# Kernel optimization log

Hardware: AMD Instinct MI355X
Metric: run time of the kernel (lower is better)

## Reference

```python
import jax, jax.numpy as jnp
import numpy as np

B, N, DIN, DOUT, H, DH, DC, NL, L = 8, 256, 64, 64, 8, 8, 64, 32, 2
SCALE = DH ** -0.5  # out_dim-per-head scaling used by both attention variants


def _ln(x, g, b):
    m = jnp.mean(x, -1, keepdims=True)
    v = jnp.mean((x - m) ** 2, -1, keepdims=True)
    return (x - m) * jax.lax.rsqrt(v + 1e-5) * g + b


def _cross_attn(x, ctx, mask_b, wq, wkv, wo, bo):
    # CrossAttentionLayer: standard softmax attention with clamp(-5,5)
    b, n, _ = x.shape
    m = ctx.shape[1]
    q = (x @ wq).reshape(b, n, H, DH).transpose(0, 2, 1, 3)
    k, v = jnp.split(ctx @ wkv, 2, axis=-1)
    k = k.reshape(b, m, H, DH).transpose(0, 2, 1, 3)
    v = v.reshape(b, m, H, DH).transpose(0, 2, 1, 3)
    sim = jnp.einsum('bhid,bhjd->bhij', q, k) * SCALE
    if mask_b is not None:
        sim = jnp.where(mask_b[:, None, None, :], sim, -jnp.finfo(sim.dtype).max)
    sim = jnp.clip(sim, -5.0, 5.0)
    attn = jax.nn.softmax(sim, axis=-1)
    out = jnp.einsum('bhij,bhjd->bhid', attn, v)
    out = out.transpose(0, 2, 1, 3).reshape(b, n, H * DH)
    return out @ wo + bo


def _mha_edge(p, e, k_RW, mask, wq, wk, we, wv):
    # GraphiT MultiHeadAttentionLayer with edge features + k_RW attention PE
    Q = (p @ wq).reshape(B, N, H, DH)
    K = (p @ wk).reshape(B, N, H, DH) * SCALE
    V = (p @ wv).reshape(B, N, H, DH).transpose(0, 2, 1, 3)  # [B,H,N,d]
    E = (e @ we).reshape(B, N, N, H, DH)
    scores = jnp.einsum('bihk,bjhk,bijhk->bhij', Q, K, E)
    scores = jnp.exp(scores - jnp.max(scores, axis=(-2, -1), keepdims=True))
    scores = scores * mask[:, None, :, None] * mask[:, None, None, :]
    scores = scores * k_RW
    denom = jnp.clip(jnp.sum(scores, -1, keepdims=True), 1e-6, None)
    out = jnp.einsum('bhij,bhjd->bhid', scores, V) / denom
    return out.transpose(0, 2, 1, 3).reshape(B, N, H * DH)


def setup_inputs() -> dict:
    key = jax.random.key(0)
    ks = jax.random.split(key, 32)
    rn = lambda k, s: jax.random.normal(k, s, dtype=jnp.float32)
    inp = {
        'h': rn(ks[0], (B, N, DIN)),
        'p': rn(ks[1], (B, N, DIN)),
        'e': rn(ks[2], (B, N, N, DIN)),
        'k_RW': jax.random.uniform(ks[3], (B, 1, N, N), dtype=jnp.float32),
        'queries': rn(ks[4], (B, NL, DC)),
        'mask': jnp.ones((B, N), dtype=jnp.float32),
        # attention_p (MultiHeadAttentionLayer) weights
        'wq_p': rn(ks[5], (DIN, H * DH)) * 0.05,
        'wk_p': rn(ks[6], (DIN, H * DH)) * 0.05,
        'we_p': rn(ks[7], (DIN, H * DH)) * 0.05,
        'wv_p': rn(ks[8], (DIN, H * DH)) * 0.05,
        'wo_p': rn(ks[9], (DOUT, DOUT)) * 0.05,
        # cross_attention_h (queries attend to nodes)
        'cq_wq': rn(ks[10], (DC, H * DH)) * 0.05,
        'cq_wkv': rn(ks[11], (DIN, 2 * H * DH)) * 0.05,
        'cq_wo': rn(ks[12], (H * DH, DC)) * 0.05,
        'cq_bo': jnp.zeros((DC,), dtype=jnp.float32),
        # L_cross latent self-attention layers (stacked)
        'sa_wq': rn(ks[13], (L, DC, H * DH)) * 0.05,
        'sa_wkv': rn(ks[14], (L, DC, 2 * H * DH)) * 0.05,
        'sa_wo': rn(ks[15], (L, H * DH, DC)) * 0.05,
        'sa_bo': jnp.zeros((L, DC), dtype=jnp.float32),
        # O_queries, norms, FFN
        'oq_w': rn(ks[16], (DC, DC)) * 0.05,
        'ln1_g': jnp.ones((DC,), dtype=jnp.float32),
        'ln1_b': jnp.zeros((DC,), dtype=jnp.float32),
        'ffn_w1': rn(ks[17], (DC, 2 * DC)) * 0.05,
        'ffn_w2': rn(ks[18], (2 * DC, DC)) * 0.05,
        'ln2_g': jnp.ones((DC,), dtype=jnp.float32),
        'ln2_b': jnp.zeros((DC,), dtype=jnp.float32),
    }
    return inp


def reference(h, p, e, k_RW, queries, mask,
              wq_p, wk_p, we_p, wv_p, wo_p,
              cq_wq, cq_wkv, cq_wo, cq_bo,
              sa_wq, sa_wkv, sa_wo, sa_bo,
              oq_w, ln1_g, ln1_b, ffn_w1, ffn_w2, ln2_g, ln2_b):
    # forward_p: update positional encoding via edge-modulated attention
    p_attn = _mha_edge(p, e, k_RW, mask, wq_p, wk_p, we_p, wv_p)
    p_new = p + jnp.tanh(p_attn @ wo_p)  # residual, no dropout (eval)
    # combine node features with updated PE (use_node_pe='sum')
    h_c = h + p_new
    mask_b = mask > 0.5
    # perceiver cross-attention: latents attend to nodes
    q = queries + _cross_attn(queries, h_c, mask_b, cq_wq, cq_wkv, cq_wo, cq_bo)
    # L_cross latent self-attention blocks with residual
    for i in range(L):
        q = q + _cross_attn(q, q, None, sa_wq[i], sa_wkv[i], sa_wo[i], sa_bo[i])
    # O_queries projection + layer norm
    q = _ln(q @ oq_w, ln1_g, ln1_b)
    # feed-forward block on queries
    ff = jax.nn.relu(q @ ffn_w1) @ ffn_w2
    q = _ln(q + ff, ln2_g, ln2_b)
    return q
```

## Files before the change

kernel.cpp:

```cpp
#include <hip/hip_runtime.h>
#include <hip/hip_bf16.h>
#include <math.h>

typedef __bf16 bf16x8 __attribute__((ext_vector_type(8)));
typedef float floatx4 __attribute__((ext_vector_type(4)));

#define ATT_SCALE 0.35355339059327373f

__device__ __forceinline__ __bf16 f2b(float x) { return (__bf16)x; }

__global__ void k_proj(const float* __restrict__ p, const float* __restrict__ quer,
                       const float* __restrict__ wq, const float* __restrict__ wk,
                       const float* __restrict__ wv, const float* __restrict__ cq_wq,
                       float* __restrict__ Q, float* __restrict__ Ks,
                       float* __restrict__ V, float* __restrict__ q1) {
  int blk = blockIdx.x, t = threadIdx.x;
  __shared__ float xr[64];
  if (blk < 2048) {
    xr[t] = p[blk * 64 + t];
    __syncthreads();
    float aq = 0.f, ak = 0.f, av = 0.f;
    for (int c = 0; c < 64; c++) {
      float x = xr[c];
      aq += x * wq[c * 64 + t];
      ak += x * wk[c * 64 + t];
      av += x * wv[c * 64 + t];
    }
    Q[blk * 64 + t] = aq;
    Ks[blk * 64 + t] = ak * ATT_SCALE;
    V[blk * 64 + t] = av;
  } else {
    int r = blk - 2048;
    xr[t] = quer[r * 64 + t];
    __syncthreads();
    float a = 0.f;
    for (int c = 0; c < 64; c++) a += xr[c] * cq_wq[c * 64 + t];
    q1[r * 64 + t] = a;
  }
}

#define LOADT(ER, JT) do {                         \
    const float* _np = ebase + (JT) * 1024;        \
    ER[0] = *(const float4*)(_np);                 \
    ER[1] = *(const float4*)(_np + 4);             \
    ER[2] = *(const float4*)(_np + 32);            \
    ER[3] = *(const float4*)(_np + 36);            \
  } while (0)

#define NTCOMP(NT, KF, VA) do {                                               \
    floatx4 acc = {0.f, 0.f, 0.f, 0.f};                                       \
    acc = __builtin_amdgcn_mfma_f32_16x16x32_bf16(wfrag[NT][0], a0, acc, 0, 0, 0); \
    acc = __builtin_amdgcn_mfma_f32_16x16x32_bf16(wfrag[NT][1], a1, acc, 0, 0, 0); \
    float s = acc[0] * KF.x * qv[NT].x + acc[1] * KF.y * qv[NT].y +           \
              acc[2] * KF.z * qv[NT].z + acc[3] * KF.w * qv[NT].w;            \
    s += __shfl_xor(s, 16);                                                   \
    float wg = __expf(s) * kwm;                                               \
    aden[NT] += wg;                                                           \
    aout[NT][0] += wg * VA.x; aout[NT][1] += wg * VA.y;                       \
    aout[NT][2] += wg * VA.z; aout[NT][3] += wg * VA.w;                       \
  } while (0)

#define STEP(JT, ER, PFSTMT) do {                                             \
    int jS = w * 64 + (JT) * 16 + l15;                                        \
    const float* ksrow = Ks + ((long)(b * 256 + jS)) * 64 + quad * 4;         \
    const float* vrow  = V  + ((long)(b * 256 + jS)) * 64 + hsel * 8 + par * 4; \
    float4 kf0 = *(const float4*)(ksrow);                                     \
    float4 kf1 = *(const float4*)(ksrow + 16);                                \
    float4 kf2 = *(const float4*)(ksrow + 32);                                \
    float4 kf3 = *(const float4*)(ksrow + 48);                                \
    float4 va0 = *(const float4*)(vrow);                                      \
    float4 va1 = *(const float4*)(vrow + 16);                                 \
    float4 va2 = *(const float4*)(vrow + 32);                                 \
    float4 va3 = *(const float4*)(vrow + 48);                                 \
    float kwm = krw[(long)bi * 256 + jS] * mask[b * 256 + jS];                \
    __builtin_amdgcn_sched_barrier(0);                                        \
    PFSTMT;                                                                   \
    __builtin_amdgcn_sched_barrier(0);                                        \
    bf16x8 a0, a1;                                                            \
    a0[0] = f2b(ER[0].x); a0[1] = f2b(ER[0].y);                               \
    a0[2] = f2b(ER[0].z); a0[3] = f2b(ER[0].w);                               \
    a0[4] = f2b(ER[1].x); a0[5] = f2b(ER[1].y);                               \
    a0[6] = f2b(ER[1].z); a0[7] = f2b(ER[1].w);                               \
    a1[0] = f2b(ER[2].x); a1[1] = f2b(ER[2].y);                               \
    a1[2] = f2b(ER[2].z); a1[3] = f2b(ER[2].w);                               \
    a1[4] = f2b(ER[3].x); a1[5] = f2b(ER[3].y);                               \
    a1[6] = f2b(ER[3].z); a1[7] = f2b(ER[3].w);                               \
    NTCOMP(0, kf0, va0); NTCOMP(1, kf1, va1);                                 \
    NTCOMP(2, kf2, va2); NTCOMP(3, kf3, va3);                                 \
  } while (0)

__global__ __launch_bounds__(256, 1) void k_edge(
    const float* __restrict__ e, const float* __restrict__ we,
    const float* __restrict__ krw, const float* __restrict__ mask,
    const float* __restrict__ hin, const float* __restrict__ pin,
    const float* __restrict__ wo, const float* __restrict__ cq_wkv,
    const float* __restrict__ Q, const float* __restrict__ Ks,
    const float* __restrict__ V, float* __restrict__ Kc, float* __restrict__ Vc) {
  int bi = blockIdx.x;
  int b = bi >> 8;
  int t = threadIdx.x;
  int w = t >> 6, l = t & 63;
  int l15 = l & 15, quad = l >> 4;
  int hsel = quad >> 1;
  int par = quad & 1;

  bf16x8 wfrag[4][2];
#pragma unroll
  for (int nt = 0; nt < 4; nt++)
#pragma unroll
    for (int kc = 0; kc < 2; kc++)
#pragma unroll
      for (int jj = 0; jj < 8; jj++)
        wfrag[nt][kc][jj] = f2b(we[(kc * 32 + quad * 8 + jj) * 64 + nt * 16 + l15]);

  float4 qv[4];
#pragma unroll
  for (int nt = 0; nt < 4; nt++)
    qv[nt] = *(const float4*)(Q + bi * 64 + nt * 16 + quad * 4);

  float mi = mask[bi];

  float aout[4][4];
  float aden[4] = {0.f, 0.f, 0.f, 0.f};
#pragma unroll
  for (int nt = 0; nt < 4; nt++)
#pragma unroll
    for (int d = 0; d < 4; d++) aout[nt][d] = 0.f;

  const float* ebase = e + ((long)bi * 256 + w * 64 + l15) * 64 + quad * 8;

  float4 e0[4], e1[4], e2[4], e3[4];
  LOADT(e0, 0);
  LOADT(e1, 1);
  LOADT(e2, 2);
  __builtin_amdgcn_sched_barrier(0);

  STEP(0, e0, LOADT(e3, 3));
  STEP(1, e1, (void)0);
  STEP(2, e2, (void)0);
  STEP(3, e3, (void)0);

#pragma unroll
  for (int nt = 0; nt < 4; nt++) {
    float dn = aden[nt];
    dn += __shfl_xor(dn, 1); dn += __shfl_xor(dn, 2);
    dn += __shfl_xor(dn, 4); dn += __shfl_xor(dn, 8);
    aden[nt] = dn;
#pragma unroll
    for (int d = 0; d < 4; d++) {
      float o = aout[nt][d];
      o += __shfl_xor(o, 1); o += __shfl_xor(o, 2);
      o += __shfl_xor(o, 4); o += __shfl_xor(o, 8);
      aout[nt][d] = o;
    }
  }

  __shared__ float red[4][64];
  __shared__ float redden[4][8];
  __shared__ float pav[64];
  __shared__ float hcl[64];
  if (l15 == 0) {
#pragma unroll
    for (int nt = 0; nt < 4; nt++) {
      int head = nt * 2 + hsel;
#pragma unroll
      for (int d = 0; d < 4; d++) red[w][head * 8 + par * 4 + d] = aout[nt][d];
      if (par == 0) redden[w][head] = aden[nt];
    }
  }
  __syncthreads();
  if (t < 64) {
    int head = t >> 3;
    float num = red[0][t] + red[1][t] + red[2][t] + red[3][t];
    float den = redden[0][head] + redden[1][head] + redden[2][head] + redden[3][head];
    num *= mi;
    den = fmaxf(den * mi, 1e-6f);
    pav[t] = num / den;
  }
  __syncthreads();
  if (t < 64) {
    float a = 0.f;
    for (int c = 0; c < 64; c++) a += pav[c] * wo[c * 64 + t];
    hcl[t] = hin[bi * 64 + t] + pin[bi * 64 + t] + tanhf(a);
  }
  __syncthreads();
  if (t < 128) {
    float a = 0.f;
    for (int c = 0; c < 64; c++) a += hcl[c] * cq_wkv[c * 128 + t];
    if (t < 64) Kc[bi * 64 + t] = a;
    else        Vc[bi * 64 + t - 64] = a;
  }
}

__global__ __launch_bounds__(256) void k_crossf(
    const float* __restrict__ q1, const float* __restrict__ Kc,
    const float* __restrict__ Vc, const float* __restrict__ mask,
    const float* __restrict__ quer, const float* __restrict__ cq_wo,
    const float* __restrict__ cq_bo, const float* __restrict__ wq0,
    const float* __restrict__ wkv0, float* __restrict__ q0g,
    float* __restrict__ qqg, float* __restrict__ kvg) {
  int blk = blockIdx.x, b = blk >> 3, rg = blk & 7;
  int t = threadIdx.x, rr = t >> 6, l = t & 63, h = l >> 3, g = l & 7;
  int gr = b * 32 + rg * 4 + rr;
  __shared__ float ocs[4][64];
  __shared__ float q0s[4][64];

  {
    const float* qp = q1 + gr * 64 + h * 8;
    float4 qa = *(const float4*)qp, qb = *(const float4*)(qp + 4);
    float num[8] = {0.f, 0.f, 0.f, 0.f, 0.f, 0.f, 0.f, 0.f};
    float den = 0.f;
#pragma unroll 4
    for (int jj = 0; jj < 32; jj++) {
      int j = jj * 8 + g;
      const float* kp = Kc + (b * 256 + j) * 64 + h * 8;
      float4 ka = *(const float4*)kp, kb = *(const float4*)(kp + 4);
      float s = qa.x * ka.x + qa.y * ka.y + qa.z * ka.z + qa.w * ka.w +
                qb.x * kb.x + qb.y * kb.y + qb.z * kb.z + qb.w * kb.w;
      s *= ATT_SCALE;
      float mj = mask[b * 256 + j];
      s = (mj > 0.5f) ? s : -1e30f;
      s = fminf(fmaxf(s, -5.f), 5.f);
      float ex = __expf(s);
      den += ex;
      const float* vp = Vc + (b * 256 + j) * 64 + h * 8;
      float4 va = *(const float4*)vp, vb = *(const float4*)(vp + 4);
      num[0] += ex * va.x; num[1] += ex * va.y;
      num[2] += ex * va.z; num[3] += ex * va.w;
      num[4] += ex * vb.x; num[5] += ex * vb.y;
      num[6] += ex * vb.z; num[7] += ex * vb.w;
    }
    den += __shfl_xor(den, 1); den += __shfl_xor(den, 2); den += __shfl_xor(den, 4);
#pragma unroll
    for (int d = 0; d < 8; d++) {
      float v = num[d];
      v += __shfl_xor(v, 1); v += __shfl_xor(v, 2); v += __shfl_xor(v, 4);
      num[d] = v;
    }
    float sel = num[0];
#pragma unroll
    for (int d = 1; d < 8; d++) sel = (g == d) ? num[d] : sel;
    ocs[rr][h * 8 + g] = sel / den;
  }

  int c = l;
  {
    float acc = quer[gr * 64 + c] + cq_bo[c];
    for (int k = 0; k < 64; k++) acc += ocs[rr][k] * cq_wo[k * 64 + c];
    q0g[gr * 64 + c] = acc;
    q0s[rr][c] = acc;
  }
  {
    float aq = 0.f, ak = 0.f, av = 0.f;
    for (int k = 0; k < 64; k++) {
      float x = q0s[rr][k];
      aq += x * wq0[k * 64 + c];
      ak += x * wkv0[k * 128 + c];
      av += x * wkv0[k * 128 + 64 + c];
    }
    qqg[gr * 64 + c] = aq;
    kvg[gr * 128 + c] = ak;
    kvg[gr * 128 + 64 + c] = av;
  }
}

__global__ __launch_bounds__(256) void k_sattnf(
    const float* __restrict__ qq, const float* __restrict__ kv,
    const float* __restrict__ resid, const float* __restrict__ wo,
    const float* __restrict__ bo, const float* __restrict__ wq2,
    const float* __restrict__ wkv2, float* __restrict__ q_out,
    float* __restrict__ qq2, float* __restrict__ kv2) {
  int blk = blockIdx.x, b = blk >> 3, rg = blk & 7;
  int t = threadIdx.x, rr = t >> 6, l = t & 63, h = l >> 3, g = l & 7;
  int gr = b * 32 + rg * 4 + rr;
  __shared__ float KVs[32][128];
  __shared__ float ocs[4][64];
  __shared__ float q2s[4][64];

  const float4* s4 = (const float4*)(kv + b * 4096);
  float4* d4 = (float4*)&KVs[0][0];
#pragma unroll
  for (int i = 0; i < 4; i++) d4[i * 256 + t] = s4[i * 256 + t];

  const float* qp = qq + gr * 64 + h * 8;
  float4 qa = *(const float4*)qp, qb = *(const float4*)(qp + 4);
  __syncthreads();

  {
    float num[8] = {0.f, 0.f, 0.f, 0.f, 0.f, 0.f, 0.f, 0.f};
    float den = 0.f;
#pragma unroll
    for (int jj = 0; jj < 4; jj++) {
      int j = jj * 8 + g;
      float4 ka = *(const float4*)&KVs[j][h * 8];
      float4 kb = *(const float4*)&KVs[j][h * 8 + 4];
      float s = qa.x * ka.x + qa.y * ka.y + qa.z * ka.z + qa.w * ka.w +
                qb.x * kb.x + qb.y * kb.y + qb.z * kb.z + qb.w * kb.w;
      s *= ATT_SCALE;
      s = fminf(fmaxf(s, -5.f), 5.f);
      float ex = __expf(s);
      den += ex;
      float4 va = *(const float4*)&KVs[j][64 + h * 8];
      float4 vb = *(const float4*)&KVs[j][64 + h * 8 + 4];
      num[0] += ex * va.x; num[1] += ex * va.y;
      num[2] += ex * va.z; num[3] += ex * va.w;
      num[4] += ex * vb.x; num[5] += ex * vb.y;
      num[6] += ex * vb.z; num[7] += ex * vb.w;
    }
    den += __shfl_xor(den, 1); den += __shfl_xor(den, 2); den += __shfl_xor(den, 4);
#pragma unroll
    for (int d = 0; d < 8; d++) {
      float v = num[d];
      v += __shfl_xor(v, 1); v += __shfl_xor(v, 2); v += __shfl_xor(v, 4);
      num[d] = v;
    }
    float sel = num[0];
#pragma unroll
    for (int d = 1; d < 8; d++) sel = (g == d) ? num[d] : sel;
    ocs[rr][h * 8 + g] = sel / den;
  }

  int c = l;
  {
    float acc = resid[gr * 64 + c] + bo[c];
    for (int k = 0; k < 64; k++) acc += ocs[rr][k] * wo[k * 64 + c];
    q_out[gr * 64 + c] = acc;
    q2s[rr][c] = acc;
  }
  {
    float aq = 0.f, ak = 0.f, av = 0.f;
    for (int k = 0; k < 64; k++) {
      float x = q2s[rr][k];
      aq += x * wq2[k * 64 + c];
      ak += x * wkv2[k * 128 + c];
      av += x * wkv2[k * 128 + 64 + c];
    }
    qq2[gr * 64 + c] = aq;
    kv2[gr * 128 + c] = ak;
    kv2[gr * 128 + 64 + c] = av;
  }
}

__global__ __launch_bounds__(256) void k_finalf(
    const float* __restrict__ qq, const float* __restrict__ kv,
    const float* __restrict__ resid, const float* __restrict__ wo,
    const float* __restrict__ bo, const float* __restrict__ oqw,
    const float* __restrict__ g1, const float* __restrict__ b1,
    const float* __restrict__ w1, const float* __restrict__ w2,
    const float* __restrict__ g2, const float* __restrict__ b2v,
    float* __restrict__ out) {
  int blk = blockIdx.x, b = blk >> 3, rg = blk & 7;
  int t = threadIdx.x, rr = t >> 6, l = t & 63, h = l >> 3, g = l & 7;
  int gr = b * 32 + rg * 4 + rr;
  __shared__ float KVs[32][128];
  __shared__ float ocs[4][64];
  __shared__ float xs[4][64];
  __shared__ float hs[4][128];

  const float4* s4 = (const float4*)(kv + b * 4096);
  float4* d4 = (float4*)&KVs[0][0];
#pragma unroll
  for (int i = 0; i < 4; i++) d4[i * 256 + t] = s4[i * 256 + t];

  const float* qp = qq + gr * 64 + h * 8;
  float4 qa = *(const float4*)qp, qb = *(const float4*)(qp + 4);
  __syncthreads();

  {
    float num[8] = {0.f, 0.f, 0.f, 0.f, 0.f, 0.f, 0.f, 0.f};
    float den = 0.f;
#pragma unroll
    for (int jj = 0; jj < 4; jj++) {
      int j = jj * 8 + g;
      float4 ka = *(const float4*)&KVs[j][h * 8];
      float4 kb = *(const float4*)&KVs[j][h * 8 + 4];
      float s = qa.x * ka.x + qa.y * ka.y + qa.z * ka.z + qa.w * ka.w +
                qb.x * kb.x + qb.y * kb.y + qb.z * kb.z + qb.w * kb.w;
      s *= ATT_SCALE;
      s = fminf(fmaxf(s, -5.f), 5.f);
      float ex = __expf(s);
      den += ex;
      float4 va = *(const float4*)&KVs[j][64 + h * 8];
      float4 vb = *(const float4*)&KVs[j][64 + h * 8 + 4];
      num[0] += ex * va.x; num[1] += ex * va.y;
      num[2] += ex * va.z; num[3] += ex * va.w;
      num[4] += ex * vb.x; num[5] += ex * vb.y;
      num[6] += ex * vb.z; num[7] += ex * vb.w;
    }
    den += __shfl_xor(den, 1); den += __shfl_xor(den, 2); den += __shfl_xor(den, 4);
#pragma unroll
    for (int d = 0; d < 8; d++) {
      float v = num[d];
      v += __shfl_xor(v, 1); v += __shfl_xor(v, 2); v += __shfl_xor(v, 4);
      num[d] = v;
    }
    float sel = num[0];
#pragma unroll
    for (int d = 1; d < 8; d++) sel = (g == d) ? num[d] : sel;
    ocs[rr][h * 8 + g] = sel / den;
  }

  int c = l;
  float y;
  {
    float acc = resid[gr * 64 + c] + bo[c];
    for (int k = 0; k < 64; k++) acc += ocs[rr][k] * wo[k * 64 + c];
    xs[rr][c] = acc;
  }
  {
    float x = 0.f;
    for (int k = 0; k < 64; k++) x += xs[rr][k] * oqw[k * 64 + c];
    float m = x;
    for (int off = 1; off < 64; off <<= 1) m += __shfl_xor(m, off);
    m *= (1.f / 64.f);
    float dv = x - m, vv = dv * dv;
    for (int off = 1; off < 64; off <<= 1) vv += __shfl_xor(vv, off);
    vv *= (1.f / 64.f);
    y = dv * rsqrtf(vv + 1e-5f) * g1[c] + b1[c];
    xs[rr][c] = y;
  }
  {
    float h1 = 0.f, h2 = 0.f;
    for (int k = 0; k < 64; k++) {
      float xx = xs[rr][k];
      h1 += xx * w1[k * 128 + c];
      h2 += xx * w1[k * 128 + 64 + c];
    }
    hs[rr][c] = fmaxf(h1, 0.f);
    hs[rr][64 + c] = fmaxf(h2, 0.f);
  }
  {
    float ff = 0.f;
    for (int k = 0; k < 128; k++) ff += hs[rr][k] * w2[k * 64 + c];
    float z = y + ff;
    float m2 = z;
    for (int off = 1; off < 64; off <<= 1) m2 += __shfl_xor(m2, off);
    m2 *= (1.f / 64.f);
    float dz = z - m2, v2 = dz * dz;
    for (int off = 1; off < 64; off <<= 1) v2 += __shfl_xor(v2, off);
    v2 *= (1.f / 64.f);
    out[gr * 64 + c] = dz * rsqrtf(v2 + 1e-5f) * g2[c] + b2v[c];
  }
}

extern "C" void kernel_launch(void* const* d_in, const int* in_sizes, int n_in,
                              void* d_out, int out_size, void* d_ws, size_t ws_size,
                              hipStream_t stream) {
  const float* h_in   = (const float*)d_in[0];
  const float* p_in   = (const float*)d_in[1];
  const float* e_in   = (const float*)d_in[2];
  const float* krw    = (const float*)d_in[3];
  const float* quer   = (const float*)d_in[4];
  const float* mask   = (const float*)d_in[5];
  const float* wq_p   = (const float*)d_in[6];
  const float* wk_p   = (const float*)d_in[7];
  const float* we_p   = (const float*)d_in[8];
  const float* wv_p   = (const float*)d_in[9];
  const float* wo_p   = (const float*)d_in[10];
  const float* cq_wq  = (const float*)d_in[11];
  const float* cq_wkv = (const float*)d_in[12];
  const float* cq_wo  = (const float*)d_in[13];
  const float* cq_bo  = (const float*)d_in[14];
  const float* sa_wq  = (const float*)d_in[15];
  const float* sa_wkv = (const float*)d_in[16];
  const float* sa_wo  = (const float*)d_in[17];
  const float* sa_bo  = (const float*)d_in[18];
  const float* oq_w   = (const float*)d_in[19];
  const float* ln1_g  = (const float*)d_in[20];
  const float* ln1_b  = (const float*)d_in[21];
  const float* ffn_w1 = (const float*)d_in[22];
  const float* ffn_w2 = (const float*)d_in[23];
  const float* ln2_g  = (const float*)d_in[24];
  const float* ln2_b  = (const float*)d_in[25];

  float* ws = (float*)d_ws;
  float* Q   = ws;
  float* Ks  = Q + 131072;
  float* V   = Ks + 131072;
  float* q1  = V + 131072;
  float* Kc  = q1 + 16384;
  float* Vc  = Kc + 131072;
  float* q0  = Vc + 131072;
  float* qc1 = q0 + 16384;
  float* qqA = qc1 + 16384;
  float* qqB = qqA + 16384;
  float* kvA = qqB + 16384;
  float* kvB = kvA + 32768;

  k_proj<<<2304, 64, 0, stream>>>(p_in, quer, wq_p, wk_p, wv_p, cq_wq, Q, Ks, V, q1);
  k_edge<<<2048, 256, 0, stream>>>(e_in, we_p, krw, mask, h_in, p_in, wo_p, cq_wkv,
                                   Q, Ks, V, Kc, Vc);
  k_crossf<<<64, 256, 0, stream>>>(q1, Kc, Vc, mask, quer, cq_wo, cq_bo,
                                   sa_wq, sa_wkv, q0, qqA, kvA);
  k_sattnf<<<64, 256, 0, stream>>>(qqA, kvA, q0, sa_wo, sa_bo,
                                   sa_wq + 4096, sa_wkv + 8192, qc1, qqB, kvB);
  k_finalf<<<64, 256, 0, stream>>>(qqB, kvB, qc1, sa_wo + 4096, sa_bo + 64, oq_w,
                                   ln1_g, ln1_b, ffn_w1, ffn_w2, ln2_g, ln2_b,
                                   (float*)d_out);
}
```

Baseline: 329.3 us.

## Split edge attention into single-wave blocks with a separate post-projection kernel

```diff
diff --git a/kernel.cpp b/kernel.cpp
--- a/kernel.cpp
+++ b/kernel.cpp
@@ -20,6 +20,7 @@
     xr[t] = p[blk * 64 + t];
     __syncthreads();
     float aq = 0.f, ak = 0.f, av = 0.f;
+#pragma unroll
     for (int c = 0; c < 64; c++) {
       float x = xr[c];
       aq += x * wq[c * 64 + t];
@@ -34,6 +35,7 @@
     xr[t] = quer[r * 64 + t];
     __syncthreads();
     float a = 0.f;
+#pragma unroll
     for (int c = 0; c < 64; c++) a += xr[c] * cq_wq[c * 64 + t];
     q1[r * 64 + t] = a;
   }
@@ -61,7 +63,7 @@
   } while (0)
 
 #define STEP(JT, ER, PFSTMT) do {                                             \
-    int jS = w * 64 + (JT) * 16 + l15;                                        \
+    int jS = qd * 64 + (JT) * 16 + l15;                                       \
     const float* ksrow = Ks + ((long)(b * 256 + jS)) * 64 + quad * 4;         \
     const float* vrow  = V  + ((long)(b * 256 + jS)) * 64 + hsel * 8 + par * 4; \
     float4 kf0 = *(const float4*)(ksrow);                                     \
@@ -89,17 +91,16 @@
     NTCOMP(2, kf2, va2); NTCOMP(3, kf3, va3);                                 \
   } while (0)
 
-__global__ __launch_bounds__(256, 1) void k_edge(
+__global__ __launch_bounds__(64, 1) void k_edge(
     const float* __restrict__ e, const float* __restrict__ we,
     const float* __restrict__ krw, const float* __restrict__ mask,
-    const float* __restrict__ hin, const float* __restrict__ pin,
-    const float* __restrict__ wo, const float* __restrict__ cq_wkv,
     const float* __restrict__ Q, const float* __restrict__ Ks,
-    const float* __restrict__ V, float* __restrict__ Kc, float* __restrict__ Vc) {
-  int bi = blockIdx.x;
+    const float* __restrict__ V, float* __restrict__ ppart,
+    float* __restrict__ pden) {
+  int gid = blockIdx.x;
+  int bi = gid >> 2, qd = gid & 3;
   int b = bi >> 8;
-  int t = threadIdx.x;
-  int w = t >> 6, l = t & 63;
+  int l = threadIdx.x;
   int l15 = l & 15, quad = l >> 4;
   int hsel = quad >> 1;
   int par = quad & 1;
@@ -118,8 +119,6 @@
   for (int nt = 0; nt < 4; nt++)
     qv[nt] = *(const float4*)(Q + bi * 64 + nt * 16 + quad * 4);
 
-  float mi = mask[bi];
-
   float aout[4][4];
   float aden[4] = {0.f, 0.f, 0.f, 0.f};
 #pragma unroll
@@ -127,7 +126,7 @@
 #pragma unroll
     for (int d = 0; d < 4; d++) aout[nt][d] = 0.f;
 
-  const float* ebase = e + ((long)bi * 256 + w * 64 + l15) * 64 + quad * 8;
+  const float* ebase = e + ((long)bi * 256 + qd * 64 + l15) * 64 + quad * 8;
 
   float4 e0[4], e1[4], e2[4], e3[4];
   LOADT(e0, 0);
@@ -155,40 +154,74 @@
     }
   }
 
-  __shared__ float red[4][64];
-  __shared__ float redden[4][8];
-  __shared__ float pav[64];
-  __shared__ float hcl[64];
   if (l15 == 0) {
 #pragma unroll
     for (int nt = 0; nt < 4; nt++) {
       int head = nt * 2 + hsel;
 #pragma unroll
-      for (int d = 0; d < 4; d++) red[w][head * 8 + par * 4 + d] = aout[nt][d];
-      if (par == 0) redden[w][head] = aden[nt];
+      for (int d = 0; d < 4; d++)
+        ppart[(long)gid * 64 + head * 8 + par * 4 + d] = aout[nt][d];
+      if (par == 0) pden[(long)gid * 8 + head] = aden[nt];
+    }
+  }
+}
+
+__global__ __launch_bounds__(256) void k_post(
+    const float* __restrict__ ppart, const float* __restrict__ pden,
+    const float* __restrict__ mask, const float* __restrict__ hin,
+    const float* __restrict__ pin, const float* __restrict__ wo,
+    const float* __restrict__ cq_wkv, float* __restrict__ Kc,
+    float* __restrict__ Vc) {
+  int r0 = blockIdx.x * 8;
+  int t = threadIdx.x;
+  __shared__ float pavs[8][64];
+  __shared__ float hcs[8][64];
+
+  {
+    int col = t & 63, rr = t >> 6;
+#pragma unroll
+    for (int k = 0; k < 2; k++) {
+      int row = r0 + rr + k * 4;
+      float num = 0.f, den = 0.f;
+#pragma unroll
+      for (int q = 0; q < 4; q++) {
+        num += ppart[(long)(row * 4 + q) * 64 + col];
+        den += pden[(long)(row * 4 + q) * 8 + (col >> 3)];
+      }
+      float mi = mask[row];
+      pavs[rr + k * 4][col] = (num * mi) / fmaxf(den * mi, 1e-6f);
     }
   }
   __syncthreads();
-  if (t < 64) {
-    int head = t >> 3;
-    float num = red[0][t] + red[1][t] + red[2][t] + red[3][t];
-    float den = redden[0][head] + redden[1][head] + redden[2][head] + redden[3][head];
-    num *= mi;
-    den = fmaxf(den * mi, 1e-6f);
-    pav[t] = num / den;
+  {
+    int col = t & 63, rr = t >> 6;
+    float a0 = 0.f, a1 = 0.f;
+#pragma unroll
+    for (int c = 0; c < 64; c++) {
+      float wv = wo[c * 64 + col];
+      a0 += pavs[rr][c] * wv;
+      a1 += pavs[rr + 4][c] * wv;
+    }
+    int row0 = r0 + rr, row1 = r0 + rr + 4;
+    hcs[rr][col] = hin[row0 * 64 + col] + pin[row0 * 64 + col] + tanhf(a0);
+    hcs[rr + 4][col] = hin[row1 * 64 + col] + pin[row1 * 64 + col] + tanhf(a1);
   }
   __syncthreads();
-  if (t < 64) {
-    float a = 0.f;
-    for (int c = 0; c < 64; c++) a += pav[c] * wo[c * 64 + t];
-    hcl[t] = hin[bi * 64 + t] + pin[bi * 64 + t] + tanhf(a);
-  }
-  __syncthreads();
-  if (t < 128) {
-    float a = 0.f;
-    for (int c = 0; c < 64; c++) a += hcl[c] * cq_wkv[c * 128 + t];
-    if (t < 64) Kc[bi * 64 + t] = a;
-    else        Vc[bi * 64 + t - 64] = a;
+  {
+    int col = t & 127, rr = t >> 7;
+    float a[4] = {0.f, 0.f, 0.f, 0.f};
+#pragma unroll
+    for (int c = 0; c < 64; c++) {
+      float wv = cq_wkv[c * 128 + col];
+#pragma unroll
+      for (int m = 0; m < 4; m++) a[m] += hcs[rr + 2 * m][c] * wv;
+    }
+#pragma unroll
+    for (int m = 0; m < 4; m++) {
+      int row = r0 + rr + 2 * m;
+      if (col < 64) Kc[row * 64 + col] = a[m];
+      else          Vc[row * 64 + col - 64] = a[m];
+    }
   }
 }
 
@@ -246,12 +279,14 @@
   int c = l;
   {
     float acc = quer[gr * 64 + c] + cq_bo[c];
+#pragma unroll
     for (int k = 0; k < 64; k++) acc += ocs[rr][k] * cq_wo[k * 64 + c];
     q0g[gr * 64 + c] = acc;
     q0s[rr][c] = acc;
   }
   {
     float aq = 0.f, ak = 0.f, av = 0.f;
+#pragma unroll
     for (int k = 0; k < 64; k++) {
       float x = q0s[rr][k];
       aq += x * wq0[k * 64 + c];
@@ -323,12 +358,14 @@
   int c = l;
   {
     float acc = resid[gr * 64 + c] + bo[c];
+#pragma unroll
     for (int k = 0; k < 64; k++) acc += ocs[rr][k] * wo[k * 64 + c];
     q_out[gr * 64 + c] = acc;
     q2s[rr][c] = acc;
   }
   {
     float aq = 0.f, ak = 0.f, av = 0.f;
+#pragma unroll
     for (int k = 0; k < 64; k++) {
       float x = q2s[rr][k];
       aq += x * wq2[k * 64 + c];
@@ -404,11 +441,13 @@
   float y;
   {
     float acc = resid[gr * 64 + c] + bo[c];
+#pragma unroll
     for (int k = 0; k < 64; k++) acc += ocs[rr][k] * wo[k * 64 + c];
     xs[rr][c] = acc;
   }
   {
     float x = 0.f;
+#pragma unroll
     for (int k = 0; k < 64; k++) x += xs[rr][k] * oqw[k * 64 + c];
     float m = x;
     for (int off = 1; off < 64; off <<= 1) m += __shfl_xor(m, off);
@@ -421,6 +460,7 @@
   }
   {
     float h1 = 0.f, h2 = 0.f;
+#pragma unroll
     for (int k = 0; k < 64; k++) {
       float xx = xs[rr][k];
       h1 += xx * w1[k * 128 + c];
@@ -431,6 +471,7 @@
   }
   {
     float ff = 0.f;
+#pragma unroll
     for (int k = 0; k < 128; k++) ff += hs[rr][k] * w2[k * 64 + c];
     float z = y + ff;
     float m2 = z;
@@ -474,22 +515,25 @@
   const float* ln2_b  = (const float*)d_in[25];
 
   float* ws = (float*)d_ws;
-  float* Q   = ws;
-  float* Ks  = Q + 131072;
-  float* V   = Ks + 131072;
-  float* q1  = V + 131072;
-  float* Kc  = q1 + 16384;
-  float* Vc  = Kc + 131072;
-  float* q0  = Vc + 131072;
-  float* qc1 = q0 + 16384;
-  float* qqA = qc1 + 16384;
-  float* qqB = qqA + 16384;
-  float* kvA = qqB + 16384;
-  float* kvB = kvA + 32768;
+  float* Q    = ws;
+  float* Ks   = Q + 131072;
+  float* V    = Ks + 131072;
+  float* q1   = V + 131072;
+  float* Kc   = q1 + 16384;
+  float* Vc   = Kc + 131072;
+  float* q0   = Vc + 131072;
+  float* qc1  = q0 + 16384;
+  float* qqA  = qc1 + 16384;
+  float* qqB  = qqA + 16384;
+  float* kvA  = qqB + 16384;
+  float* kvB  = kvA + 32768;
+  float* ppart = kvB + 32768;
+  float* pden  = ppart + 524288;
 
   k_proj<<<2304, 64, 0, stream>>>(p_in, quer, wq_p, wk_p, wv_p, cq_wq, Q, Ks, V, q1);
-  k_edge<<<2048, 256, 0, stream>>>(e_in, we_p, krw, mask, h_in, p_in, wo_p, cq_wkv,
-                                   Q, Ks, V, Kc, Vc);
+  k_edge<<<8192, 64, 0, stream>>>(e_in, we_p, krw, mask, Q, Ks, V, ppart, pden);
+  k_post<<<256, 256, 0, stream>>>(ppart, pden, mask, h_in, p_in, wo_p, cq_wkv,
+                                  Kc, Vc);
   k_crossf<<<64, 256, 0, stream>>>(q1, Kc, Vc, mask, quer, cq_wo, cq_bo,
                                    sa_wq, sa_wkv, q0, qqA, kvA);
   k_sattnf<<<64, 256, 0, stream>>>(qqA, kvA, q0, sa_wo, sa_bo,
```

Result: slower. 354.3 us (+7.6%).

## Stage edge tile through swizzled bf16 LDS with coalesced loads; unroll GEMV loops

Applied to the files above, without the earlier changes.

```diff
diff --git a/kernel.cpp b/kernel.cpp
--- a/kernel.cpp
+++ b/kernel.cpp
@@ -20,6 +20,7 @@
     xr[t] = p[blk * 64 + t];
     __syncthreads();
     float aq = 0.f, ak = 0.f, av = 0.f;
+#pragma unroll
     for (int c = 0; c < 64; c++) {
       float x = xr[c];
       aq += x * wq[c * 64 + t];
@@ -34,18 +35,11 @@
     xr[t] = quer[r * 64 + t];
     __syncthreads();
     float a = 0.f;
+#pragma unroll
     for (int c = 0; c < 64; c++) a += xr[c] * cq_wq[c * 64 + t];
     q1[r * 64 + t] = a;
   }
 }
-
-#define LOADT(ER, JT) do {                         \
-    const float* _np = ebase + (JT) * 1024;        \
-    ER[0] = *(const float4*)(_np);                 \
-    ER[1] = *(const float4*)(_np + 4);             \
-    ER[2] = *(const float4*)(_np + 32);            \
-    ER[3] = *(const float4*)(_np + 36);            \
-  } while (0)
 
 #define NTCOMP(NT, KF, VA) do {                                               \
     floatx4 acc = {0.f, 0.f, 0.f, 0.f};                                       \
@@ -60,8 +54,11 @@
     aout[NT][2] += wg * VA.z; aout[NT][3] += wg * VA.w;                       \
   } while (0)
 
-#define STEP(JT, ER, PFSTMT) do {                                             \
+#define STEP8(JT) do {                                                        \
     int jS = w * 64 + (JT) * 16 + l15;                                        \
+    const __bf16* rp = &elds[jS * 64];                                        \
+    bf16x8 a0 = *reinterpret_cast<const bf16x8*>(rp + ((quad ^ (l15 & 7)) * 8)); \
+    bf16x8 a1 = *reinterpret_cast<const bf16x8*>(rp + (((quad + 4) ^ (l15 & 7)) * 8)); \
     const float* ksrow = Ks + ((long)(b * 256 + jS)) * 64 + quad * 4;         \
     const float* vrow  = V  + ((long)(b * 256 + jS)) * 64 + hsel * 8 + par * 4; \
     float4 kf0 = *(const float4*)(ksrow);                                     \
@@ -73,18 +70,6 @@
     float4 va2 = *(const float4*)(vrow + 32);                                 \
     float4 va3 = *(const float4*)(vrow + 48);                                 \
     float kwm = krw[(long)bi * 256 + jS] * mask[b * 256 + jS];                \
-    __builtin_amdgcn_sched_barrier(0);                                        \
-    PFSTMT;                                                                   \
-    __builtin_amdgcn_sched_barrier(0);                                        \
-    bf16x8 a0, a1;                                                            \
-    a0[0] = f2b(ER[0].x); a0[1] = f2b(ER[0].y);                               \
-    a0[2] = f2b(ER[0].z); a0[3] = f2b(ER[0].w);                               \
-    a0[4] = f2b(ER[1].x); a0[5] = f2b(ER[1].y);                               \
-    a0[6] = f2b(ER[1].z); a0[7] = f2b(ER[1].w);                               \
-    a1[0] = f2b(ER[2].x); a1[1] = f2b(ER[2].y);                               \
-    a1[2] = f2b(ER[2].z); a1[3] = f2b(ER[2].w);                               \
-    a1[4] = f2b(ER[3].x); a1[5] = f2b(ER[3].y);                               \
-    a1[6] = f2b(ER[3].z); a1[7] = f2b(ER[3].w);                               \
     NTCOMP(0, kf0, va0); NTCOMP(1, kf1, va1);                                 \
     NTCOMP(2, kf2, va2); NTCOMP(3, kf3, va3);                                 \
   } while (0)
@@ -104,6 +89,35 @@
   int hsel = quad >> 1;
   int par = quad & 1;
 
+  __shared__ __align__(16) __bf16 elds[256 * 64];
+  __shared__ float red[4][64];
+  __shared__ float redden[4][8];
+  __shared__ float pav[64];
+  __shared__ float hcl[64];
+
+  int srow = t >> 3;
+  int scg = t & 7;
+  const float* esrc = e + ((long)bi * 256 + srow) * 64 + scg * 8;
+  float4 s0[8], s1[8];
+#pragma unroll
+  for (int k = 0; k < 8; k++) {
+    const float* p = esrc + 2048L * k;
+    s0[k] = *(const float4*)p;
+    s1[k] = *(const float4*)(p + 4);
+  }
+  __builtin_amdgcn_sched_barrier(0);
+
+#pragma unroll
+  for (int k = 0; k < 8; k++) {
+    int row = srow + 32 * k;
+    int g = scg ^ (row & 7);
+    bf16x8 v;
+    v[0] = f2b(s0[k].x); v[1] = f2b(s0[k].y); v[2] = f2b(s0[k].z); v[3] = f2b(s0[k].w);
+    v[4] = f2b(s1[k].x); v[5] = f2b(s1[k].y); v[6] = f2b(s1[k].z); v[7] = f2b(s1[k].w);
+    *reinterpret_cast<bf16x8*>(&elds[row * 64 + g * 8]) = v;
+  }
+  __builtin_amdgcn_sched_barrier(0);
+
   bf16x8 wfrag[4][2];
 #pragma unroll
   for (int nt = 0; nt < 4; nt++)
@@ -127,18 +141,12 @@
 #pragma unroll
     for (int d = 0; d < 4; d++) aout[nt][d] = 0.f;
 
-  const float* ebase = e + ((long)bi * 256 + w * 64 + l15) * 64 + quad * 8;
-
-  float4 e0[4], e1[4], e2[4], e3[4];
-  LOADT(e0, 0);
-  LOADT(e1, 1);
-  LOADT(e2, 2);
-  __builtin_amdgcn_sched_barrier(0);
-
-  STEP(0, e0, LOADT(e3, 3));
-  STEP(1, e1, (void)0);
-  STEP(2, e2, (void)0);
-  STEP(3, e3, (void)0);
+  __syncthreads();
+
+  STEP8(0);
+  STEP8(1);
+  STEP8(2);
+  STEP8(3);
 
 #pragma unroll
   for (int nt = 0; nt < 4; nt++) {
@@ -155,10 +163,6 @@
     }
   }
 
-  __shared__ float red[4][64];
-  __shared__ float redden[4][8];
-  __shared__ float pav[64];
-  __shared__ float hcl[64];
   if (l15 == 0) {
 #pragma unroll
     for (int nt = 0; nt < 4; nt++) {
@@ -180,12 +184,14 @@
   __syncthreads();
   if (t < 64) {
     float a = 0.f;
+#pragma unroll
     for (int c = 0; c < 64; c++) a += pav[c] * wo[c * 64 + t];
     hcl[t] = hin[bi * 64 + t] + pin[bi * 64 + t] + tanhf(a);
   }
   __syncthreads();
   if (t < 128) {
     float a = 0.f;
+#pragma unroll
     for (int c = 0; c < 64; c++) a += hcl[c] * cq_wkv[c * 128 + t];
     if (t < 64) Kc[bi * 64 + t] = a;
     else        Vc[bi * 64 + t - 64] = a;
@@ -246,12 +252,14 @@
   int c = l;
   {
     float acc = quer[gr * 64 + c] + cq_bo[c];
+#pragma unroll
     for (int k = 0; k < 64; k++) acc += ocs[rr][k] * cq_wo[k * 64 + c];
     q0g[gr * 64 + c] = acc;
     q0s[rr][c] = acc;
   }
   {
     float aq = 0.f, ak = 0.f, av = 0.f;
+#pragma unroll
     for (int k = 0; k < 64; k++) {
       float x = q0s[rr][k];
       aq += x * wq0[k * 64 + c];
@@ -323,12 +331,14 @@
   int c = l;
   {
     float acc = resid[gr * 64 + c] + bo[c];
+#pragma unroll
     for (int k = 0; k < 64; k++) acc += ocs[rr][k] * wo[k * 64 + c];
     q_out[gr * 64 + c] = acc;
     q2s[rr][c] = acc;
   }
   {
     float aq = 0.f, ak = 0.f, av = 0.f;
+#pragma unroll
     for (int k = 0; k < 64; k++) {
       float x = q2s[rr][k];
       aq += x * wq2[k * 64 + c];
@@ -404,11 +414,13 @@
   float y;
   {
     float acc = resid[gr * 64 + c] + bo[c];
+#pragma unroll
     for (int k = 0; k < 64; k++) acc += ocs[rr][k] * wo[k * 64 + c];
     xs[rr][c] = acc;
   }
   {
     float x = 0.f;
+#pragma unroll
     for (int k = 0; k < 64; k++) x += xs[rr][k] * oqw[k * 64 + c];
     float m = x;
     for (int off = 1; off < 64; off <<= 1) m += __shfl_xor(m, off);
@@ -421,6 +433,7 @@
   }
   {
     float h1 = 0.f, h2 = 0.f;
+#pragma unroll
     for (int k = 0; k < 64; k++) {
       float xx = xs[rr][k];
       h1 += xx * w1[k * 128 + c];
@@ -431,6 +444,7 @@
   }
   {
     float ff = 0.f;
+#pragma unroll
     for (int k = 0; k < 128; k++) ff += hs[rr][k] * w2[k * 64 + c];
     float z = y + ff;
     float m2 = z;
```

New measurement: 359.0 us. 9.0% more time.
